# Kernel optimization log

Hardware: AMD Instinct MI355X
Metric: run time of the kernel (lower is better)

## Reference

```python
import jax, jax.numpy as jnp
import numpy as np


def _pairwise_dist(x):
    # Euclidean (p=2) pairwise distances via Gram identity; avoids the
    # [N, N, D] broadcasted difference tensor the torch code materializes.
    sq = jnp.sum(x * x, axis=1)                      # [N]
    d2 = sq[:, None] + sq[None, :] - 2.0 * (x @ x.T)  # [N, N]
    return jnp.sqrt(jnp.clip(d2, 0.0))


def _persistence_pairs(dist_np):
    """0-dim persistent homology pairs = MST edges via Kruskal union-find,
    processed in order of increasing edge weight (matches the repo's
    PersistentHomologyCalculation). Returns [N-1, 2] int64 index pairs."""
    n = dist_np.shape[0]
    iu, ju = np.triu_indices(n, k=1)
    order = np.argsort(dist_np[iu, ju], kind='stable')
    parent = np.arange(n)

    def find(i):
        root = i
        while parent[root] != root:
            root = parent[root]
        while parent[i] != root:  # path compression
            parent[i], i = root, parent[i]
        return root

    pairs = []
    for e in order:
        a, b = find(iu[e]), find(ju[e])
        if a != b:
            parent[a] = b
            pairs.append((iu[e], ju[e]))
            if len(pairs) == n - 1:
                break
    return np.asarray(pairs, dtype=np.int64)


def setup_inputs() -> dict:
    key = jax.random.key(0)
    x = jax.random.normal(key, (2048, 4096), dtype=jnp.float32)
    return {"x": x}


def reference(x):
    distances = _pairwise_dist(x)  # [N, N]
    # Pair selection is done on host on detached values, as in the original
    # (pairs have fixed count N-1, so the output shape is static).
    pairs = _persistence_pairs(np.asarray(jax.device_get(distances)))
    i = jnp.asarray(pairs[:, 0])
    j = jnp.asarray(pairs[:, 1])
    selected_distances = distances[i, j]  # [N-1]
    return selected_distances
```

## Files before the change

### kernel.cpp

```cpp
#include <hip/hip_runtime.h>
#include <stdint.h>

#define NPTS 2048
#define KDIM 4096
#define INVALID_KEY 0xFFFFFFFFFFFFFFFFull

typedef __bf16 bf16x8 __attribute__((ext_vector_type(8)));
typedef float f32x4 __attribute__((ext_vector_type(4)));

__device__ __forceinline__ unsigned short f2bf(float f) {
    unsigned int u = __float_as_uint(f);
    u = (u + 0x7FFFu + ((u >> 16) & 1u)) >> 16;
    return (unsigned short)u;
}

__device__ __forceinline__ void gld_lds16(const unsigned short* g, unsigned short* l) {
    __builtin_amdgcn_global_load_lds(
        (const __attribute__((address_space(1))) unsigned int*)g,
        (__attribute__((address_space(3))) unsigned int*)l, 16, 0, 0);
}

__device__ __forceinline__ unsigned long long mk_key(float w, int i, int j) {
    unsigned long long a = (i < j) ? i : j;
    unsigned long long b = (i < j) ? j : i;
    return ((unsigned long long)__float_as_uint(w) << 22) | (a << 11) | b;
}

__global__ __launch_bounds__(256) void convert_sqnorm_kernel(const float* __restrict__ x,
                                                             unsigned short* __restrict__ xb,
                                                             float* __restrict__ sq,
                                                             int* __restrict__ comp0,
                                                             unsigned long long* __restrict__ best0,
                                                             int* __restrict__ ctl) {
    const int row = blockIdx.x;
    const float* xr = x + (size_t)row * KDIM;
    unsigned short* xbr = xb + (size_t)row * KDIM;
    const int t = threadIdx.x;
    float s = 0.f;
    #pragma unroll
    for (int k = 0; k < 4; ++k) {
        int c = t * 4 + k * 1024;
        float4 v = *(const float4*)(xr + c);
        s += v.x * v.x + v.y * v.y + v.z * v.z + v.w * v.w;
        uint2 u;
        u.x = (unsigned)f2bf(v.x) | ((unsigned)f2bf(v.y) << 16);
        u.y = (unsigned)f2bf(v.z) | ((unsigned)f2bf(v.w) << 16);
        *(uint2*)(xbr + c) = u;
    }
    for (int off = 32; off; off >>= 1) s += __shfl_down(s, off);
    __shared__ float p[4];
    if ((t & 63) == 0) p[t >> 6] = s;
    __syncthreads();
    if (t == 0) {
        sq[row] = p[0] + p[1] + p[2] + p[3];
        comp0[row] = row;
        best0[row] = INVALID_KEY;
        if (row == 0) { ctl[0] = 0; ctl[1] = 0; }
    }
}

__global__ __launch_bounds__(256, 2) void gemm_d2_glds(const unsigned short* __restrict__ xb,
                                                       const float* __restrict__ sq,
                                                       float* __restrict__ D2,
                                                       unsigned long long* __restrict__ best0) {
    __shared__ __align__(16) unsigned short tile[2 * 12288];
    const int I0 = blockIdx.y * 64;
    const int J0 = blockIdx.x * 128;
    const int t = threadIdx.x;
    const int lane = t & 63;
    const int w = t >> 6;
    const int m = lane & 15, q = lane >> 4;

    const int rp = lane >> 2;
    const int sg = (lane & 3) ^ ((lane >> 3) & 3);
    const unsigned short* gsrc[6]; int ldoff[6];
    #pragma unroll
    for (int s = 0; s < 2; ++s)
        #pragma unroll
        for (int ci = 0; ci < 3; ++ci) {
            int c = w * 3 + ci;
            int rowbase = (c < 4) ? (I0 + c * 16) : (J0 + (c - 4) * 16);
            int idx = s * 3 + ci;
            gsrc[idx] = xb + (size_t)(rowbase + rp) * KDIM + s * 32 + sg * 8;
            ldoff[idx] = (s * 12 + c) * 512;
        }
    const int fro = m * 32 + ((q ^ ((m >> 1) & 3)) * 8);

    f32x4 acc[4][2] = {};
    unsigned short* buf0 = tile;
    unsigned short* buf1 = tile + 12288;

    auto STAGE = [&](unsigned short* base, int kc) {
        #pragma unroll
        for (int idx = 0; idx < 6; ++idx)
            gld_lds16(gsrc[idx] + kc, base + ldoff[idx]);
    };
    auto COMPUTE = [&](const unsigned short* base) {
        #pragma unroll
        for (int s = 0; s < 2; ++s) {
            bf16x8 af[4], bg[2];
            #pragma unroll
            for (int rt = 0; rt < 4; ++rt)
                af[rt] = *(const bf16x8*)(base + (s * 12 + rt) * 512 + fro);
            #pragma unroll
            for (int ct = 0; ct < 2; ++ct)
                bg[ct] = *(const bf16x8*)(base + (s * 12 + 4 + w * 2 + ct) * 512 + fro);
            #pragma unroll
            for (int rt = 0; rt < 4; ++rt)
                #pragma unroll
                for (int ct = 0; ct < 2; ++ct)
                    acc[rt][ct] = __builtin_amdgcn_mfma_f32_16x16x32_bf16(
                        af[rt], bg[ct], acc[rt][ct], 0, 0, 0);
        }
    };

    STAGE(buf0, 0);
    __syncthreads();
    #pragma unroll 1
    for (int kc = 64; kc < KDIM - 64; kc += 128) {
        STAGE(buf1, kc);
        COMPUTE(buf0);
        __syncthreads();
        STAGE(buf0, kc + 64);
        COMPUTE(buf1);
        __syncthreads();
    }
    STAGE(buf1, KDIM - 64);
    COMPUTE(buf0);
    __syncthreads();
    COMPUTE(buf1);
    __syncthreads();

    unsigned long long* s_best = (unsigned long long*)tile;
    if (t < 64) s_best[t] = INVALID_KEY;
    __syncthreads();
    #pragma unroll
    for (int rt = 0; rt < 4; ++rt) {
        #pragma unroll
        for (int r = 0; r < 4; ++r) {
            int i = I0 + rt * 16 + q * 4 + r;
            unsigned long long kk = INVALID_KEY;
            #pragma unroll
            for (int ct = 0; ct < 2; ++ct) {
                int j = J0 + w * 32 + ct * 16 + m;
                float v = sq[i] + sq[j] - 2.0f * acc[rt][ct][r];
                v = (i == j) ? __builtin_inff() : fmaxf(v, 0.0f);
                D2[(size_t)i * NPTS + j] = v;
                if (i != j) {
                    unsigned long long key = mk_key(v, i, j);
                    kk = (key < kk) ? key : kk;
                }
            }
            #pragma unroll
            for (int mask = 1; mask < 16; mask <<= 1) {
                unsigned long long o = __shfl_xor(kk, mask);
                kk = (o < kk) ? o : kk;
            }
            if (m == 0) atomicMin(&s_best[rt * 16 + q * 4 + r], kk);
        }
    }
    __syncthreads();
    if (t < 64) atomicMin(&best0[I0 + t], s_best[t]);
}

__global__ __launch_bounds__(256) void boruvka_round(const float* __restrict__ D2,
                                                     const unsigned long long* __restrict__ bestP,
                                                     unsigned long long* __restrict__ bestN,
                                                     const int* __restrict__ compP,
                                                     int* __restrict__ compN,
                                                     float* __restrict__ ew,
                                                     int* __restrict__ ctl) {
    if (ctl[1]) return;
    __shared__ int sc[NPTS];
    __shared__ unsigned long long compBest[NPTS];
    __shared__ int par[NPTS];
    __shared__ int s_wsum[4];
    __shared__ int s_nroots;
    const int t = threadIdx.x;
    const int bid = blockIdx.x;
    const int lane = t & 63, w = t >> 6;

    if (t == 0) s_nroots = 0;
    #pragma unroll
    for (int e = 0; e < 8; ++e) {
        int v = t * 8 + e;
        sc[v] = compP[v];
        compBest[v] = INVALID_KEY;
    }
    __syncthreads();

    unsigned long long kreg[8]; int oreg[8];
    #pragma unroll
    for (int e = 0; e < 8; ++e) {
        int v = t * 8 + e;
        unsigned long long k = bestP[v];
        kreg[e] = k;
        int a = (int)((k >> 11) & 2047), b = (int)(k & 2047);
        oreg[e] = (a == v) ? b : a;
        if (k != INVALID_KEY && sc[oreg[e]] != sc[v])
            atomicMin(&compBest[sc[v]], k);
    }
    __syncthreads();

    bool isr[8];
    #pragma unroll
    for (int e = 0; e < 8; ++e) {
        int c = t * 8 + e;
        int p = c;
        isr[e] = (sc[c] == c);
        if (isr[e]) {
            unsigned long long k = compBest[c];
            if (k != INVALID_KEY) {
                int a = (int)((k >> 11) & 2047), b = (int)(k & 2047);
                int j = (sc[a] == c) ? b : a;
                int rj = sc[j];
                bool mutual = (compBest[rj] == k);
                if (!(mutual && c < rj)) {
                    p = rj;
                    if (bid == 0)
                        ew[atomicAdd(&ctl[0], 1)] = __uint_as_float((unsigned)(k >> 22));
                }
            }
        }
        par[c] = p;
    }
    int any = __syncthreads_or(1);
    do {
        int local = 0;
        #pragma unroll
        for (int e = 0; e < 8; ++e) {
            if (isr[e]) {
                int c = t * 8 + e;
                int p = par[c];
                int np = par[p];
                if (np != p) { par[c] = np; local = 1; }
            }
        }
        any = __syncthreads_or(local);
    } while (any);

    int newsc[8]; int rc = 0;
    #pragma unroll
    for (int e = 0; e < 8; ++e) {
        int v = t * 8 + e;
        newsc[e] = par[sc[v]];
        if (newsc[e] == v) rc++;
    }
    if (rc) atomicAdd(&s_nroots, rc);
    __syncthreads();
    #pragma unroll
    for (int e = 0; e < 8; ++e) sc[t * 8 + e] = newsc[e];
    __syncthreads();
    const int nroots = s_nroots;

    if (bid == 0) {
        #pragma unroll
        for (int e = 0; e < 8; ++e) compN[t * 8 + e] = newsc[e];
        if (t == 0 && nroots == 1) ctl[1] = 1;
    }
    if (nroots == 1) return;

    int flags[8], lc = 0;
    #pragma unroll
    for (int e = 0; e < 8; ++e) {
        int v = t * 8 + e;
        flags[e] = (kreg[e] == INVALID_KEY) || (sc[oreg[e]] == sc[v]);
        lc += flags[e];
    }
    int scn = lc;
    #pragma unroll
    for (int d = 1; d < 64; d <<= 1) {
        int o = __shfl_up(scn, d);
        if (lane >= d) scn += o;
    }
    if (lane == 63) s_wsum[w] = scn;
    __syncthreads();
    int wbase = 0;
    for (int i = 0; i < w; ++i) wbase += s_wsum[i];
    const int cnt = s_wsum[0] + s_wsum[1] + s_wsum[2] + s_wsum[3];
    int base = wbase + scn - lc;
    int* rlist = par;
    #pragma unroll
    for (int e = 0; e < 8; ++e)
        if (flags[e]) rlist[base++] = t * 8 + e;
    __syncthreads();

    if (t < 4) {
        int v = bid * 4 + t;
        unsigned long long k = bestP[v];
        if (k != INVALID_KEY) {
            int a = (int)((k >> 11) & 2047), b = (int)(k & 2047);
            int o = (a == v) ? b : a;
            if (sc[o] != sc[v]) bestN[v] = k;
        }
    }
    int widx = bid * 4 + w;
    if (widx < cnt) {
        int v = rlist[widx];
        int mc = sc[v];
        const float* row = D2 + (size_t)v * NPTS;
        unsigned long long best = INVALID_KEY;
        #pragma unroll
        for (int k = 0; k < 8; ++k) {
            int j0 = k * 256 + lane * 4;
            float4 w4 = *(const float4*)(row + j0);
            int4 c4 = *(const int4*)(sc + j0);
            float wa[4] = {w4.x, w4.y, w4.z, w4.w};
            int ca[4] = {c4.x, c4.y, c4.z, c4.w};
            #pragma unroll
            for (int e = 0; e < 4; ++e) {
                if (ca[e] != mc) {
                    unsigned long long key = mk_key(wa[e], v, j0 + e);
                    best = (key < best) ? key : best;
                }
            }
        }
        for (int off = 32; off; off >>= 1) {
            unsigned long long o = __shfl_down(best, off);
            best = (o < best) ? o : best;
        }
        if (lane == 0) bestN[v] = best;
    }
}

__global__ __launch_bounds__(1024) void sort_out_kernel(const float* __restrict__ ew,
                                                        float* __restrict__ out) {
    __shared__ float wl[NPTS];
    const int t = threadIdx.x;
    for (int i = t; i < NPTS; i += 1024)
        wl[i] = (i < NPTS - 1) ? ew[i] : __builtin_inff();
    __syncthreads();
    for (int k = 2; k <= NPTS; k <<= 1) {
        for (int j = k >> 1; j > 0; j >>= 1) {
            for (int i = t; i < NPTS; i += 1024) {
                int l = i ^ j;
                if (l > i) {
                    float a = wl[i], b = wl[l];
                    bool up = ((i & k) == 0);
                    if ((a > b) == up) { wl[i] = b; wl[l] = a; }
                }
            }
            __syncthreads();
        }
    }
    for (int i = t; i < NPTS - 1; i += 1024)
        out[i] = sqrtf(fmaxf(wl[i], 0.0f));
}

extern "C" void kernel_launch(void* const* d_in, const int* in_sizes, int n_in,
                              void* d_out, int out_size, void* d_ws, size_t ws_size,
                              hipStream_t stream) {
    const float* x = (const float*)d_in[0];
    float* out = (float*)d_out;
    char* ws = (char*)d_ws;
    unsigned short* xb = (unsigned short*)ws;
    float* D2 = (float*)(ws + 16777216);
    size_t o = 33554432;
    float* sq = (float*)(ws + o);                  o += 8192;
    unsigned long long* best0 = (unsigned long long*)(ws + o); o += 16384;
    unsigned long long* best1 = (unsigned long long*)(ws + o); o += 16384;
    int* comp0 = (int*)(ws + o);                   o += 8192;
    int* comp1 = (int*)(ws + o);                   o += 8192;
    float* ew = (float*)(ws + o);                  o += 8192;
    int* ctl = (int*)(ws + o);

    hipLaunchKernelGGL(convert_sqnorm_kernel, dim3(NPTS), dim3(256), 0, stream,
                       x, xb, sq, comp0, best0, ctl);
    hipLaunchKernelGGL(gemm_d2_glds, dim3(16, 32), dim3(256), 0, stream,
                       xb, sq, D2, best0);
    for (int r = 0; r < 11; ++r) {
        unsigned long long* bp = (r & 1) ? best1 : best0;
        unsigned long long* bn = (r & 1) ? best0 : best1;
        int* cp = (r & 1) ? comp1 : comp0;
        int* cn = (r & 1) ? comp0 : comp1;
        hipLaunchKernelGGL(boruvka_round, dim3(512), dim3(256), 0, stream,
                           D2, bp, bn, cp, cn, ew, ctl);
    }
    hipLaunchKernelGGL(sort_out_kernel, dim3(1), dim3(1024), 0, stream, ew, out);
}
```

Baseline: 218.2 us.

## Fuse Boruvka rounds into one cooperative kernel with grid-wide sync

Replaces the 11 separate boruvka_round launches with one cooperative kernel that loops over rounds and uses grid.sync() between them. Each block keeps its component labels in shared memory across rounds instead of reloading them from global memory, and the early-exit control flag is gone. This removes per-round launch overhead and the idle tail launches that still ran after convergence. In exchange it requires all 512 blocks to be co-resident and pays for a grid barrier each round.

```diff
diff --git a/kernel.cpp b/kernel.cpp
--- a/kernel.cpp
+++ b/kernel.cpp
@@ -1,5 +1,8 @@
 #include <hip/hip_runtime.h>
+#include <hip/hip_cooperative_groups.h>
 #include <stdint.h>
+
+namespace cg = cooperative_groups;
 
 #define NPTS 2048
 #define KDIM 4096
@@ -163,14 +166,12 @@
     if (t < 64) atomicMin(&best0[I0 + t], s_best[t]);
 }
 
-__global__ __launch_bounds__(256) void boruvka_round(const float* __restrict__ D2,
-                                                     const unsigned long long* __restrict__ bestP,
-                                                     unsigned long long* __restrict__ bestN,
-                                                     const int* __restrict__ compP,
-                                                     int* __restrict__ compN,
+__global__ __launch_bounds__(256) void boruvka_fused(const float* __restrict__ D2,
+                                                     unsigned long long* __restrict__ bA,
+                                                     unsigned long long* __restrict__ bB,
                                                      float* __restrict__ ew,
                                                      int* __restrict__ ctl) {
-    if (ctl[1]) return;
+    cg::grid_group grid = cg::this_grid();
     __shared__ int sc[NPTS];
     __shared__ unsigned long long compBest[NPTS];
     __shared__ int par[NPTS];
@@ -180,146 +181,147 @@
     const int bid = blockIdx.x;
     const int lane = t & 63, w = t >> 6;
 
-    if (t == 0) s_nroots = 0;
     #pragma unroll
-    for (int e = 0; e < 8; ++e) {
-        int v = t * 8 + e;
-        sc[v] = compP[v];
-        compBest[v] = INVALID_KEY;
-    }
-    __syncthreads();
-
-    unsigned long long kreg[8]; int oreg[8];
-    #pragma unroll
-    for (int e = 0; e < 8; ++e) {
-        int v = t * 8 + e;
-        unsigned long long k = bestP[v];
-        kreg[e] = k;
-        int a = (int)((k >> 11) & 2047), b = (int)(k & 2047);
-        oreg[e] = (a == v) ? b : a;
-        if (k != INVALID_KEY && sc[oreg[e]] != sc[v])
-            atomicMin(&compBest[sc[v]], k);
-    }
-    __syncthreads();
-
-    bool isr[8];
-    #pragma unroll
-    for (int e = 0; e < 8; ++e) {
-        int c = t * 8 + e;
-        int p = c;
-        isr[e] = (sc[c] == c);
-        if (isr[e]) {
-            unsigned long long k = compBest[c];
+    for (int e = 0; e < 8; ++e) sc[t * 8 + e] = t * 8 + e;
+
+    unsigned long long* bp = bA;
+    unsigned long long* bn = bB;
+
+    #pragma unroll 1
+    for (int round = 0; round < 11; ++round) {
+        if (t == 0) s_nroots = 0;
+        #pragma unroll
+        for (int e = 0; e < 8; ++e) compBest[t * 8 + e] = INVALID_KEY;
+        __syncthreads();
+
+        unsigned long long kreg[8]; int oreg[8];
+        #pragma unroll
+        for (int e = 0; e < 8; ++e) {
+            int v = t * 8 + e;
+            unsigned long long k = bp[v];
+            kreg[e] = k;
+            int a = (int)((k >> 11) & 2047), b = (int)(k & 2047);
+            oreg[e] = (a == v) ? b : a;
+            if (k != INVALID_KEY && sc[oreg[e]] != sc[v])
+                atomicMin(&compBest[sc[v]], k);
+        }
+        __syncthreads();
+
+        bool isr[8];
+        #pragma unroll
+        for (int e = 0; e < 8; ++e) {
+            int c = t * 8 + e;
+            int p = c;
+            isr[e] = (sc[c] == c);
+            if (isr[e]) {
+                unsigned long long k = compBest[c];
+                if (k != INVALID_KEY) {
+                    int a = (int)((k >> 11) & 2047), b = (int)(k & 2047);
+                    int j = (sc[a] == c) ? b : a;
+                    int rj = sc[j];
+                    bool mutual = (compBest[rj] == k);
+                    if (!(mutual && c < rj)) {
+                        p = rj;
+                        if (bid == 0)
+                            ew[atomicAdd(&ctl[0], 1)] = __uint_as_float((unsigned)(k >> 22));
+                    }
+                }
+            }
+            par[c] = p;
+        }
+        int any = __syncthreads_or(1);
+        do {
+            int local = 0;
+            #pragma unroll
+            for (int e = 0; e < 8; ++e) {
+                if (isr[e]) {
+                    int c = t * 8 + e;
+                    int p = par[c];
+                    int np = par[p];
+                    if (np != p) { par[c] = np; local = 1; }
+                }
+            }
+            any = __syncthreads_or(local);
+        } while (any);
+
+        int newsc[8]; int rc = 0;
+        #pragma unroll
+        for (int e = 0; e < 8; ++e) {
+            int v = t * 8 + e;
+            newsc[e] = par[sc[v]];
+            if (newsc[e] == v) rc++;
+        }
+        if (rc) atomicAdd(&s_nroots, rc);
+        __syncthreads();
+        #pragma unroll
+        for (int e = 0; e < 8; ++e) sc[t * 8 + e] = newsc[e];
+        __syncthreads();
+        const int nroots = s_nroots;
+        if (nroots == 1) break;
+
+        int flags[8], lc = 0;
+        #pragma unroll
+        for (int e = 0; e < 8; ++e) {
+            int v = t * 8 + e;
+            flags[e] = (kreg[e] == INVALID_KEY) || (sc[oreg[e]] == sc[v]);
+            lc += flags[e];
+        }
+        int scn = lc;
+        #pragma unroll
+        for (int d = 1; d < 64; d <<= 1) {
+            int o = __shfl_up(scn, d);
+            if (lane >= d) scn += o;
+        }
+        if (lane == 63) s_wsum[w] = scn;
+        __syncthreads();
+        int wbase = 0;
+        for (int i = 0; i < w; ++i) wbase += s_wsum[i];
+        const int cnt = s_wsum[0] + s_wsum[1] + s_wsum[2] + s_wsum[3];
+        int base = wbase + scn - lc;
+        int* rlist = par;
+        #pragma unroll
+        for (int e = 0; e < 8; ++e)
+            if (flags[e]) rlist[base++] = t * 8 + e;
+        __syncthreads();
+
+        if (t < 4) {
+            int v = bid * 4 + t;
+            unsigned long long k = bp[v];
             if (k != INVALID_KEY) {
                 int a = (int)((k >> 11) & 2047), b = (int)(k & 2047);
-                int j = (sc[a] == c) ? b : a;
-                int rj = sc[j];
-                bool mutual = (compBest[rj] == k);
-                if (!(mutual && c < rj)) {
-                    p = rj;
-                    if (bid == 0)
-                        ew[atomicAdd(&ctl[0], 1)] = __uint_as_float((unsigned)(k >> 22));
-                }
-            }
-        }
-        par[c] = p;
-    }
-    int any = __syncthreads_or(1);
-    do {
-        int local = 0;
-        #pragma unroll
-        for (int e = 0; e < 8; ++e) {
-            if (isr[e]) {
-                int c = t * 8 + e;
-                int p = par[c];
-                int np = par[p];
-                if (np != p) { par[c] = np; local = 1; }
-            }
-        }
-        any = __syncthreads_or(local);
-    } while (any);
-
-    int newsc[8]; int rc = 0;
-    #pragma unroll
-    for (int e = 0; e < 8; ++e) {
-        int v = t * 8 + e;
-        newsc[e] = par[sc[v]];
-        if (newsc[e] == v) rc++;
-    }
-    if (rc) atomicAdd(&s_nroots, rc);
-    __syncthreads();
-    #pragma unroll
-    for (int e = 0; e < 8; ++e) sc[t * 8 + e] = newsc[e];
-    __syncthreads();
-    const int nroots = s_nroots;
-
-    if (bid == 0) {
-        #pragma unroll
-        for (int e = 0; e < 8; ++e) compN[t * 8 + e] = newsc[e];
-        if (t == 0 && nroots == 1) ctl[1] = 1;
-    }
-    if (nroots == 1) return;
-
-    int flags[8], lc = 0;
-    #pragma unroll
-    for (int e = 0; e < 8; ++e) {
-        int v = t * 8 + e;
-        flags[e] = (kreg[e] == INVALID_KEY) || (sc[oreg[e]] == sc[v]);
-        lc += flags[e];
-    }
-    int scn = lc;
-    #pragma unroll
-    for (int d = 1; d < 64; d <<= 1) {
-        int o = __shfl_up(scn, d);
-        if (lane >= d) scn += o;
-    }
-    if (lane == 63) s_wsum[w] = scn;
-    __syncthreads();
-    int wbase = 0;
-    for (int i = 0; i < w; ++i) wbase += s_wsum[i];
-    const int cnt = s_wsum[0] + s_wsum[1] + s_wsum[2] + s_wsum[3];
-    int base = wbase + scn - lc;
-    int* rlist = par;
-    #pragma unroll
-    for (int e = 0; e < 8; ++e)
-        if (flags[e]) rlist[base++] = t * 8 + e;
-    __syncthreads();
-
-    if (t < 4) {
-        int v = bid * 4 + t;
-        unsigned long long k = bestP[v];
-        if (k != INVALID_KEY) {
-            int a = (int)((k >> 11) & 2047), b = (int)(k & 2047);
-            int o = (a == v) ? b : a;
-            if (sc[o] != sc[v]) bestN[v] = k;
-        }
-    }
-    int widx = bid * 4 + w;
-    if (widx < cnt) {
-        int v = rlist[widx];
-        int mc = sc[v];
-        const float* row = D2 + (size_t)v * NPTS;
-        unsigned long long best = INVALID_KEY;
-        #pragma unroll
-        for (int k = 0; k < 8; ++k) {
-            int j0 = k * 256 + lane * 4;
-            float4 w4 = *(const float4*)(row + j0);
-            int4 c4 = *(const int4*)(sc + j0);
-            float wa[4] = {w4.x, w4.y, w4.z, w4.w};
-            int ca[4] = {c4.x, c4.y, c4.z, c4.w};
-            #pragma unroll
-            for (int e = 0; e < 4; ++e) {
-                if (ca[e] != mc) {
-                    unsigned long long key = mk_key(wa[e], v, j0 + e);
-                    best = (key < best) ? key : best;
-                }
-            }
-        }
-        for (int off = 32; off; off >>= 1) {
-            unsigned long long o = __shfl_down(best, off);
-            best = (o < best) ? o : best;
-        }
-        if (lane == 0) bestN[v] = best;
+                int o = (a == v) ? b : a;
+                if (sc[o] != sc[v]) bn[v] = k;
+            }
+        }
+        int widx = bid * 4 + w;
+        if (widx < cnt) {
+            int v = rlist[widx];
+            int mc = sc[v];
+            const float* row = D2 + (size_t)v * NPTS;
+            unsigned long long best = INVALID_KEY;
+            #pragma unroll
+            for (int k = 0; k < 8; ++k) {
+                int j0 = k * 256 + lane * 4;
+                float4 w4 = *(const float4*)(row + j0);
+                int4 c4 = *(const int4*)(sc + j0);
+                float wa[4] = {w4.x, w4.y, w4.z, w4.w};
+                int ca[4] = {c4.x, c4.y, c4.z, c4.w};
+                #pragma unroll
+                for (int e = 0; e < 4; ++e) {
+                    if (ca[e] != mc) {
+                        unsigned long long key = mk_key(wa[e], v, j0 + e);
+                        best = (key < best) ? key : best;
+                    }
+                }
+            }
+            for (int off = 32; off; off >>= 1) {
+                unsigned long long o = __shfl_down(best, off);
+                best = (o < best) ? o : best;
+            }
+            if (lane == 0) bn[v] = best;
+        }
+        grid.sync();
+        unsigned long long* tmp = bp; bp = bn; bn = tmp;
     }
 }
 
@@ -363,18 +365,17 @@
     int* comp1 = (int*)(ws + o);                   o += 8192;
     float* ew = (float*)(ws + o);                  o += 8192;
     int* ctl = (int*)(ws + o);
+    (void)comp1;
 
     hipLaunchKernelGGL(convert_sqnorm_kernel, dim3(NPTS), dim3(256), 0, stream,
                        x, xb, sq, comp0, best0, ctl);
     hipLaunchKernelGGL(gemm_d2_glds, dim3(16, 32), dim3(256), 0, stream,
                        xb, sq, D2, best0);
-    for (int r = 0; r < 11; ++r) {
-        unsigned long long* bp = (r & 1) ? best1 : best0;
-        unsigned long long* bn = (r & 1) ? best0 : best1;
-        int* cp = (r & 1) ? comp1 : comp0;
-        int* cn = (r & 1) ? comp0 : comp1;
-        hipLaunchKernelGGL(boruvka_round, dim3(512), dim3(256), 0, stream,
-                           D2, bp, bn, cp, cn, ew, ctl);
+    {
+        void* args[] = {(void*)&D2, (void*)&best0, (void*)&best1,
+                        (void*)&ew, (void*)&ctl};
+        hipLaunchCooperativeKernel((const void*)boruvka_fused, dim3(512), dim3(256),
+                                   args, 0, stream);
     }
     hipLaunchKernelGGL(sort_out_kernel, dim3(1), dim3(1024), 0, stream, ew, out);
 }
```

Result: slower. 358.2 us (+64.2%).

## Exploit distance symmetry in GEMM, dedupe component atomics, deepen pointer jumping

Applied to the files above, without the earlier changes.

The distance GEMM now launches only the upper-triangular tile set (272 blocks instead of 512). Each block writes both D2[i,j] and the transposed D2[j,i] and updates the per-point best key for both rows and columns, cutting the GEMM arithmetic roughly in half. In the Boruvka round, per-thread candidate keys aimed at the same component are merged before the shared atomicMin, and pointer jumping follows four hops per iteration instead of two. The transposed stores are strided, 16-byte writes, and the extra column reduction plus atomics add epilogue cost.

```diff
diff --git a/kernel.cpp b/kernel.cpp
--- a/kernel.cpp
+++ b/kernel.cpp
@@ -64,8 +64,15 @@
                                                        float* __restrict__ D2,
                                                        unsigned long long* __restrict__ best0) {
     __shared__ __align__(16) unsigned short tile[2 * 12288];
-    const int I0 = blockIdx.y * 64;
-    const int J0 = blockIdx.x * 128;
+    int n = blockIdx.x, by = 0, bx = 0;
+    #pragma unroll 1
+    for (int y = 0; y < 32; ++y) {
+        int wdt = 16 - (y >> 1);
+        if (n < wdt) { by = y; bx = (y >> 1) + n; break; }
+        n -= wdt;
+    }
+    const int I0 = by * 64;
+    const int J0 = bx * 128;
     const int t = threadIdx.x;
     const int lane = t & 63;
     const int w = t >> 6;
@@ -132,25 +139,37 @@
     __syncthreads();
 
     unsigned long long* s_best = (unsigned long long*)tile;
+    unsigned long long* s_bestJ = ((unsigned long long*)tile) + 64;
     if (t < 64) s_best[t] = INVALID_KEY;
-    __syncthreads();
+    if (t < 128) s_bestJ[t] = INVALID_KEY;
+    __syncthreads();
+    unsigned long long ckk[2] = {INVALID_KEY, INVALID_KEY};
     #pragma unroll
     for (int rt = 0; rt < 4; ++rt) {
-        #pragma unroll
-        for (int r = 0; r < 4; ++r) {
-            int i = I0 + rt * 16 + q * 4 + r;
-            unsigned long long kk = INVALID_KEY;
-            #pragma unroll
-            for (int ct = 0; ct < 2; ++ct) {
-                int j = J0 + w * 32 + ct * 16 + m;
+        unsigned long long rowk[4] = {INVALID_KEY, INVALID_KEY, INVALID_KEY, INVALID_KEY};
+        #pragma unroll
+        for (int ct = 0; ct < 2; ++ct) {
+            const int j = J0 + w * 32 + ct * 16 + m;
+            float tv[4];
+            #pragma unroll
+            for (int r = 0; r < 4; ++r) {
+                const int i = I0 + rt * 16 + q * 4 + r;
                 float v = sq[i] + sq[j] - 2.0f * acc[rt][ct][r];
                 v = (i == j) ? __builtin_inff() : fmaxf(v, 0.0f);
+                tv[r] = v;
                 D2[(size_t)i * NPTS + j] = v;
                 if (i != j) {
                     unsigned long long key = mk_key(v, i, j);
-                    kk = (key < kk) ? key : kk;
+                    rowk[r] = (key < rowk[r]) ? key : rowk[r];
+                    ckk[ct] = (key < ckk[ct]) ? key : ckk[ct];
                 }
             }
+            *(float4*)(D2 + (size_t)j * NPTS + (I0 + rt * 16 + q * 4)) =
+                make_float4(tv[0], tv[1], tv[2], tv[3]);
+        }
+        #pragma unroll
+        for (int r = 0; r < 4; ++r) {
+            unsigned long long kk = rowk[r];
             #pragma unroll
             for (int mask = 1; mask < 16; mask <<= 1) {
                 unsigned long long o = __shfl_xor(kk, mask);
@@ -159,8 +178,16 @@
             if (m == 0) atomicMin(&s_best[rt * 16 + q * 4 + r], kk);
         }
     }
+    #pragma unroll
+    for (int ct = 0; ct < 2; ++ct) {
+        unsigned long long ck = ckk[ct];
+        unsigned long long o = __shfl_xor(ck, 16); ck = (o < ck) ? o : ck;
+        o = __shfl_xor(ck, 32);                    ck = (o < ck) ? o : ck;
+        if (q == 0) atomicMin(&s_bestJ[w * 32 + ct * 16 + m], ck);
+    }
     __syncthreads();
     if (t < 64) atomicMin(&best0[I0 + t], s_best[t]);
+    if (t < 128) atomicMin(&best0[J0 + t], s_bestJ[t]);
 }
 
 __global__ __launch_bounds__(256) void boruvka_round(const float* __restrict__ D2,
@@ -190,6 +217,7 @@
     __syncthreads();
 
     unsigned long long kreg[8]; int oreg[8];
+    int cA[8]; unsigned long long kA[8]; bool live[8];
     #pragma unroll
     for (int e = 0; e < 8; ++e) {
         int v = t * 8 + e;
@@ -197,9 +225,21 @@
         kreg[e] = k;
         int a = (int)((k >> 11) & 2047), b = (int)(k & 2047);
         oreg[e] = (a == v) ? b : a;
-        if (k != INVALID_KEY && sc[oreg[e]] != sc[v])
-            atomicMin(&compBest[sc[v]], k);
-    }
+        cA[e] = sc[v];
+        kA[e] = k;
+        live[e] = (k != INVALID_KEY) && (sc[oreg[e]] != sc[v]);
+    }
+    #pragma unroll
+    for (int e = 1; e < 8; ++e)
+        #pragma unroll
+        for (int f = 0; f < e; ++f)
+            if (live[e] && live[f] && cA[f] == cA[e]) {
+                kA[f] = (kA[e] < kA[f]) ? kA[e] : kA[f];
+                live[e] = false;
+            }
+    #pragma unroll
+    for (int e = 0; e < 8; ++e)
+        if (live[e]) atomicMin(&compBest[cA[e]], kA[e]);
     __syncthreads();
 
     bool isr[8];
@@ -231,9 +271,11 @@
         for (int e = 0; e < 8; ++e) {
             if (isr[e]) {
                 int c = t * 8 + e;
-                int p = par[c];
-                int np = par[p];
-                if (np != p) { par[c] = np; local = 1; }
+                int p1 = par[c];
+                int p2 = par[p1];
+                int p3 = par[p2];
+                int p4 = par[p3];
+                if (p4 != p1) { par[c] = p4; local = 1; }
             }
         }
         any = __syncthreads_or(local);
@@ -366,7 +408,7 @@
 
     hipLaunchKernelGGL(convert_sqnorm_kernel, dim3(NPTS), dim3(256), 0, stream,
                        x, xb, sq, comp0, best0, ctl);
-    hipLaunchKernelGGL(gemm_d2_glds, dim3(16, 32), dim3(256), 0, stream,
+    hipLaunchKernelGGL(gemm_d2_glds, dim3(272), dim3(256), 0, stream,
                        xb, sq, D2, best0);
     for (int r = 0; r < 11; ++r) {
         unsigned long long* bp = (r & 1) ? best1 : best0;
```

After: 242.2 us. 11.0% more time.
